# Performance work log

Measured on AMD Instinct MI355X. Metric: run time of the kernel, lower is better.

## Reference

```python
import jax, jax.numpy as jnp
from jax import lax
import numpy as np

B = 128      # graphs
L = 128      # nodes (tokens) per graph
N = B * L    # total nodes
E = 262144   # edges (avg degree 16)
VOCAB = 50000
EMB = 300
H = 256      # lstm hidden per direction
GCN = 512
NCLS = 2
EPS = 1e-12


def lstm_dir(x, wih, whh, b, reverse):
    # x: [B, L, EMB]; wih: [4H, EMB]; whh: [4H, H]; b: [4H]
    bsz, seq, _ = x.shape
    hdim = whh.shape[1]
    xs = jnp.einsum('ble,ge->blg', x, wih) + b  # [B, L, 4H]
    if reverse:
        xs = xs[:, ::-1]
    def step(carry, xt):
        h, c = carry
        gates = xt + h @ whh.T
        i, f, g, o = jnp.split(gates, 4, axis=-1)  # torch gate order i,f,g,o
        i = jax.nn.sigmoid(i); f = jax.nn.sigmoid(f)
        g = jnp.tanh(g); o = jax.nn.sigmoid(o)
        c = f * c + i * g
        h = o * jnp.tanh(c)
        return (h, c), h
    h0 = jnp.zeros((bsz, hdim), x.dtype)
    _, hs = lax.scan(step, (h0, h0), jnp.swapaxes(xs, 0, 1))
    hs = jnp.swapaxes(hs, 0, 1)  # [B, L, H]
    if reverse:
        hs = hs[:, ::-1]
    return hs


def sage_conv(x, src, dst, Wl, bl, Wr):
    # PyG SAGEConv(mean, normalize=True): lin_l(mean_j x_j) + lin_r(x_i), then L2-normalize
    msg = x[src]                                              # [E, d] gather
    agg = jax.ops.segment_sum(msg, dst, num_segments=x.shape[0])
    cnt = jax.ops.segment_sum(jnp.ones((src.shape[0], 1), x.dtype), dst,
                              num_segments=x.shape[0])
    agg = agg / jnp.maximum(cnt, 1.0)
    out = agg @ Wl + bl + x @ Wr
    nrm = jnp.linalg.norm(out, axis=-1, keepdims=True)
    return out / jnp.maximum(nrm, EPS)


def setup_inputs() -> dict:
    key = jax.random.key(0)
    ks = jax.random.split(key, 24)
    word_seq = jax.random.randint(ks[0], (B, L), 0, VOCAB)
    # intra-graph edges: local endpoints + graph offset
    el = jax.random.randint(ks[1], (2, E), 0, L)
    gid = jnp.repeat(jnp.arange(E // (E // B) * 0 + B), E // B)  # [E]
    edge_index = el + gid[None, :] * L
    batch = jnp.repeat(jnp.arange(B), L)
    s = 0.05
    inp = {
        'word_seq': word_seq, 'edge_index': edge_index, 'batch': batch,
        'embed_table': jax.random.normal(ks[2], (VOCAB, EMB), jnp.float32) * 0.1,
        'wih_f': jax.random.normal(ks[3], (4 * H, EMB), jnp.float32) * s,
        'whh_f': jax.random.normal(ks[4], (4 * H, H), jnp.float32) * s,
        'b_f': jax.random.normal(ks[5], (4 * H,), jnp.float32) * s,
        'wih_b': jax.random.normal(ks[6], (4 * H, EMB), jnp.float32) * s,
        'whh_b': jax.random.normal(ks[7], (4 * H, H), jnp.float32) * s,
        'b_b': jax.random.normal(ks[8], (4 * H,), jnp.float32) * s,
        'Wl1': jax.random.normal(ks[9], (2 * H, GCN), jnp.float32) * s,
        'Wr1': jax.random.normal(ks[10], (2 * H, GCN), jnp.float32) * s,
        'b1': jnp.zeros((GCN,), jnp.float32),
        'Wl2': jax.random.normal(ks[11], (GCN, 512), jnp.float32) * s,
        'Wr2': jax.random.normal(ks[12], (GCN, 512), jnp.float32) * s,
        'b2': jnp.zeros((512,), jnp.float32),
        'Wl3': jax.random.normal(ks[13], (512, 512), jnp.float32) * s,
        'Wr3': jax.random.normal(ks[14], (512, 512), jnp.float32) * s,
        'b3': jnp.zeros((512,), jnp.float32),
        'Wlin': jax.random.normal(ks[15], (512, NCLS), jnp.float32) * s,
        'blin': jnp.zeros((NCLS,), jnp.float32),
    }
    return inp


def reference(word_seq, edge_index, batch, embed_table,
              wih_f, whh_f, b_f, wih_b, whh_b, b_b,
              Wl1, Wr1, b1, Wl2, Wr2, b2, Wl3, Wr3, b3, Wlin, blin):
    # embedding (frozen) over padded per-graph sequences; uniform lengths -> plain reshape
    xe = embed_table[word_seq]                       # [B, L, EMB]
    hf = lstm_dir(xe, wih_f, whh_f, b_f, reverse=False)
    hb = lstm_dir(xe, wih_b, whh_b, b_b, reverse=True)
    x = jnp.concatenate([hf, hb], axis=-1).reshape(N, 2 * H)  # node features
    src, dst = edge_index[0], edge_index[1]
    x = jax.nn.relu(sage_conv(x, src, dst, Wl1, b1, Wr1))
    x = jax.nn.relu(sage_conv(x, src, dst, Wl2, b2, Wr2))
    x = jax.nn.relu(sage_conv(x, src, dst, Wl3, b3, Wr3))
    # global mean pool over graphs
    s = jax.ops.segment_sum(x, batch, num_segments=B)
    c = jax.ops.segment_sum(jnp.ones((N, 1), x.dtype), batch, num_segments=B)
    pooled = s / jnp.maximum(c, 1.0)
    return pooled @ Wlin + blin                      # [B, NCLS]
```

## Files before the change

### kernel.cpp

```cpp
#include <hip/hip_runtime.h>
#include <math.h>

#define NN   16384
#define EE   262144

typedef __attribute__((ext_vector_type(8))) short  short8v;
typedef __attribute__((ext_vector_type(4))) float  f32x4;

__device__ inline unsigned short f2bf(float f) {
    union { float f; unsigned u; } v; v.f = f;
    unsigned r = v.u + 0x7fff + ((v.u >> 16) & 1);
    return (unsigned short)(r >> 16);
}
__device__ inline float bf2f(unsigned short b) {
    unsigned u = ((unsigned)b) << 16;
    union { unsigned u; float f; } v; v.u = u; return v.f;
}
__device__ inline float sigm_f(float x) { return 1.f / (1.f + __expf(-x)); }
__device__ inline float tanh_f(float x) {
    x = fminf(15.f, fmaxf(-15.f, x));
    float e = __expf(2.f * x);
    return (e - 1.f) / (e + 1.f);
}
__device__ inline int gate_orig(int np) {
    int wp = np >> 6, g = (np >> 4) & 3, jj = np & 15;
    return g * 256 + wp * 16 + jj;
}

__global__ void k_init(unsigned long long* __restrict__ hx, int* __restrict__ deg,
                       int* __restrict__ fill) {
    int i = blockIdx.x * 256 + threadIdx.x;
    if (i < 65536) hx[i] = 0ull;
    if (i < NN) { deg[i] = 0; fill[i] = 0; }
}

__global__ void k_embed_bf(const int* __restrict__ wseq, const float* __restrict__ tab,
                           unsigned short* __restrict__ xeb) {
    int i = blockIdx.x * 256 + threadIdx.x;
    if (i >= NN * 320) return;
    int row = i / 320, k = i - row * 320;
    float f = (k < 300) ? tab[wseq[row] * 300 + k] : 0.f;
    xeb[i] = f2bf(f);
}

__global__ void k_cvt_wih(const float* __restrict__ wih, unsigned short* __restrict__ wt) {
    int i = blockIdx.x * 256 + threadIdx.x;
    if (i >= 1024 * 320) return;
    int np = i / 320, k = i - np * 320;
    wt[i] = f2bf(k < 300 ? wih[gate_orig(np) * 300 + k] : 0.f);
}
__global__ void k_cvt_whh(const float* __restrict__ whh, unsigned short* __restrict__ wp) {
    int i = blockIdx.x * 256 + threadIdx.x;
    if (i >= 1024 * 256) return;
    int np = i >> 8, k = i & 255;
    wp[i] = f2bf(whh[gate_orig(np) * 256 + k]);
}
__global__ void k_permb(const float* __restrict__ b, float* __restrict__ pb) {
    int i = blockIdx.x * 256 + threadIdx.x;
    if (i < 1024) pb[i] = b[gate_orig(i)];
}
__global__ void k_cvt_wcat(const float* __restrict__ Wl, const float* __restrict__ Wr,
                           unsigned short* __restrict__ wc) {
    int i = blockIdx.x * 256 + threadIdx.x;
    if (i >= 512 * 1024) return;
    int n = i >> 10, k = i & 1023;
    float f = (k < 512) ? Wl[k * 512 + n] : Wr[(k - 512) * 512 + n];
    wc[i] = f2bf(f);
}

__global__ __launch_bounds__(256)
void k_mgemm(const unsigned short* __restrict__ A, const unsigned short* __restrict__ Bt,
             const float* __restrict__ bias, float* __restrict__ C, int N, int Ka)
{
    __shared__ unsigned short As[128 * 32];
    __shared__ unsigned short Bs[128 * 32];
    const int tid = threadIdx.x;
    const int m0 = blockIdx.x << 7, n0 = blockIdx.y << 7;
    const int w = tid >> 6, lane = tid & 63;
    const int wr = w >> 1, wc = w & 1;
    const int lr = lane & 15, lhi = lane >> 4;
    const int r0 = tid >> 2, kc0 = (tid & 3) * 8;

    f32x4 acc[4][4] = {};

    for (int k0 = 0; k0 < Ka; k0 += 32) {
        short8v a0 = *(const short8v*)(A + (m0 + r0) * Ka + k0 + kc0);
        short8v a1 = *(const short8v*)(A + (m0 + 64 + r0) * Ka + k0 + kc0);
        short8v b0 = *(const short8v*)(Bt + (n0 + r0) * Ka + k0 + kc0);
        short8v b1 = *(const short8v*)(Bt + (n0 + 64 + r0) * Ka + k0 + kc0);
        __syncthreads();
        *(short8v*)&As[r0 * 32 + kc0]        = a0;
        *(short8v*)&As[(64 + r0) * 32 + kc0] = a1;
        *(short8v*)&Bs[r0 * 32 + kc0]        = b0;
        *(short8v*)&Bs[(64 + r0) * 32 + kc0] = b1;
        __syncthreads();
        short8v af[4], bf[4];
        #pragma unroll
        for (int i = 0; i < 4; ++i)
            af[i] = *(const short8v*)&As[(wr * 64 + i * 16 + lr) * 32 + lhi * 8];
        #pragma unroll
        for (int j = 0; j < 4; ++j)
            bf[j] = *(const short8v*)&Bs[(wc * 64 + j * 16 + lr) * 32 + lhi * 8];
        #pragma unroll
        for (int i = 0; i < 4; ++i)
            #pragma unroll
            for (int j = 0; j < 4; ++j)
                acc[i][j] = __builtin_amdgcn_mfma_f32_16x16x32_bf16(af[i], bf[j], acc[i][j], 0, 0, 0);
    }
    #pragma unroll
    for (int i = 0; i < 4; ++i) {
        int row = m0 + wr * 64 + i * 16 + lhi * 4;
        #pragma unroll
        for (int j = 0; j < 4; ++j) {
            int col = n0 + wc * 64 + j * 16 + lr;
            float bv = bias[col];
            #pragma unroll
            for (int r = 0; r < 4; ++r)
                C[(row + r) * N + col] = acc[i][j][r] + bv;
        }
    }
}

__global__ __launch_bounds__(512, 2)
void k_lstm(const float* __restrict__ xs_f, const float* __restrict__ xs_b,
            const unsigned short* __restrict__ whhp_f, const unsigned short* __restrict__ whhp_b,
            unsigned short* __restrict__ xout, unsigned long long* __restrict__ hx)
{
    const int tid  = threadIdx.x;
    const int wv   = tid >> 6, lane = tid & 63;
    const int lr   = lane & 15, lh = lane >> 4;
    const int wgid = blockIdx.x;
    const int dir  = wgid >> 4;
    const int bs   = (wgid >> 1) & 7;
    const int H    = wgid & 1;
    const int b0   = bs * 16;
    const float* xs = dir ? xs_b : xs_f;
    const unsigned short* whhp = dir ? whhp_b : whhp_f;

    short8v wf[4][8];
    #pragma unroll
    for (int g = 0; g < 4; ++g)
        #pragma unroll
        for (int ks = 0; ks < 8; ++ks)
            wf[g][ks] = *(const short8v*)(whhp
                + (size_t)(H * 512 + wv * 64 + g * 16 + lr) * 256 + ks * 32 + lh * 8);

    __shared__ unsigned short At[2][16 * 256];

    unsigned long long* hx_own =
        hx + (size_t)(((dir * 8 + bs) * 2 + H) * 2) * 1024;
    const unsigned long long* hx_peer =
        hx + (size_t)(((dir * 8 + bs) * 2 + (1 - H)) * 2) * 1024;

    const int jmine = H * 128 + wv * 16 + lr;
    const int rowb  = 4 * lh;
    const int up_j    = (1 - H) * 128 + (tid >> 2);
    const int up_rowb = 4 * (tid & 3);
    const int xcol    = H * 512 + wv * 64 + lr;

    float c[4] = {0.f, 0.f, 0.f, 0.f};
    float xv[4][4];
    {
        const int l0 = dir ? 127 : 0;
        #pragma unroll
        for (int r = 0; r < 4; ++r) {
            const float* xp = xs + ((size_t)(b0 + rowb + r) * 128 + l0) * 1024 + xcol;
            #pragma unroll
            for (int g = 0; g < 4; ++g) xv[g][r] = xp[g * 16];
        }
    }

    for (int t = 0; t < 128; ++t) {
        const int l = dir ? (127 - t) : t;
        f32x4 acc[4] = {};
        if (t > 0) {
            const char* Ab = (const char*)&At[(t - 1) & 1][0];
            #pragma unroll
            for (int ks = 0; ks < 8; ++ks) {
                int off = (lr * 512 + ks * 64 + lh * 16) ^ ((lr & 7) << 4);
                short8v a = *(const short8v*)(Ab + off);
                #pragma unroll
                for (int g = 0; g < 4; ++g)
                    acc[g] = __builtin_amdgcn_mfma_f32_16x16x32_bf16(a, wf[g][ks], acc[g], 0, 0, 0);
            }
        }
        unsigned short hb[4];
        #pragma unroll
        for (int r = 0; r < 4; ++r) {
            float gi = sigm_f(acc[0][r] + xv[0][r]);
            float gf = sigm_f(acc[1][r] + xv[1][r]);
            float gg = tanh_f(acc[2][r] + xv[2][r]);
            float go = sigm_f(acc[3][r] + xv[3][r]);
            c[r] = gf * c[r] + gi * gg;
            float h = go * tanh_f(c[r]);
            hb[r] = f2bf(h);
            xout[((size_t)(b0 + rowb + r) * 128 + l) * 512 + dir * 256 + jmine] = hb[r];
        }
        if (t < 127) {
            const int p = t & 1;
            char* Aw = (char*)&At[p][0];
            #pragma unroll
            for (int r = 0; r < 4; ++r) {
                int row = rowb + r;
                int off = (row * 512 + 2 * jmine) ^ ((row & 7) << 4);
                *(unsigned short*)(Aw + off) = hb[r];
            }
            const unsigned tg = (unsigned)(t + 1);
            unsigned long long w0 = ((unsigned long long)tg << 32)
                                  | ((unsigned)hb[0] | ((unsigned)hb[1] << 16));
            unsigned long long w1 = ((unsigned long long)tg << 32)
                                  | ((unsigned)hb[2] | ((unsigned)hb[3] << 16));
            const int Wb = (wv * 16 + lr) * 8 + 2 * lh;
            __hip_atomic_store(hx_own + (size_t)p * 1024 + Wb,     w0,
                               __ATOMIC_RELAXED, __HIP_MEMORY_SCOPE_AGENT);
            __hip_atomic_store(hx_own + (size_t)p * 1024 + Wb + 1, w1,
                               __ATOMIC_RELAXED, __HIP_MEMORY_SCOPE_AGENT);
            const int l2 = dir ? (126 - t) : (t + 1);
            #pragma unroll
            for (int r = 0; r < 4; ++r) {
                const float* xp = xs + ((size_t)(b0 + rowb + r) * 128 + l2) * 1024 + xcol;
                #pragma unroll
                for (int g = 0; g < 4; ++g) xv[g][r] = xp[g * 16];
            }
            const unsigned long long* pp = hx_peer + (size_t)p * 1024 + 2 * tid;
            unsigned long long u0 = __hip_atomic_load(pp,     __ATOMIC_RELAXED, __HIP_MEMORY_SCOPE_AGENT);
            unsigned long long u1 = __hip_atomic_load(pp + 1, __ATOMIC_RELAXED, __HIP_MEMORY_SCOPE_AGENT);
            while ((unsigned)(u0 >> 32) != tg)
                u0 = __hip_atomic_load(pp,     __ATOMIC_RELAXED, __HIP_MEMORY_SCOPE_AGENT);
            while ((unsigned)(u1 >> 32) != tg)
                u1 = __hip_atomic_load(pp + 1, __ATOMIC_RELAXED, __HIP_MEMORY_SCOPE_AGENT);
            {
                int r0_ = up_rowb, r1_ = up_rowb + 1, r2_ = up_rowb + 2, r3_ = up_rowb + 3;
                *(unsigned short*)(Aw + ((r0_ * 512 + 2 * up_j) ^ ((r0_ & 7) << 4))) =
                    (unsigned short)(u0 & 0xffff);
                *(unsigned short*)(Aw + ((r1_ * 512 + 2 * up_j) ^ ((r1_ & 7) << 4))) =
                    (unsigned short)((u0 >> 16) & 0xffff);
                *(unsigned short*)(Aw + ((r2_ * 512 + 2 * up_j) ^ ((r2_ & 7) << 4))) =
                    (unsigned short)(u1 & 0xffff);
                *(unsigned short*)(Aw + ((r3_ * 512 + 2 * up_j) ^ ((r3_ & 7) << 4))) =
                    (unsigned short)((u1 >> 16) & 0xffff);
            }
            __syncthreads();
        }
    }
}

__global__ void k_hist(const int* __restrict__ ei, int* __restrict__ deg) {
    int e = blockIdx.x * 256 + threadIdx.x;
    if (e >= EE) return;
    atomicAdd(&deg[ei[EE + e]], 1);
}

__global__ void k_scan(const int* __restrict__ deg, int* __restrict__ indptr) {
    __shared__ int sm[256];
    int tid = threadIdx.x;
    int b0 = tid * 64;
    int s = 0;
    for (int i = 0; i < 64; ++i) s += deg[b0 + i];
    sm[tid] = s;
    __syncthreads();
    for (int off = 1; off < 256; off <<= 1) {
        int v = (tid >= off) ? sm[tid - off] : 0;
        __syncthreads();
        sm[tid] += v;
        __syncthreads();
    }
    int run = sm[tid] - s;
    for (int i = 0; i < 64; ++i) { indptr[b0 + i] = run; run += deg[b0 + i]; }
    if (tid == 255) indptr[NN] = run;
}

__global__ void k_scatter(const int* __restrict__ ei, const int* __restrict__ indptr,
                          int* __restrict__ fill, int* __restrict__ cols) {
    int e = blockIdx.x * 256 + threadIdx.x;
    if (e >= EE) return;
    int d = ei[EE + e];
    int slot = atomicAdd(&fill[d], 1);
    cols[indptr[d] + slot] = ei[e];
}

__global__ __launch_bounds__(256)
void k_gather_bf(const unsigned short* __restrict__ x, const int* __restrict__ indptr,
                 const int* __restrict__ cols, unsigned short* __restrict__ catb)
{
    int gw = (blockIdx.x * 256 + threadIdx.x) >> 6;
    int lane = threadIdx.x & 63;
    if (gw >= NN) return;
    int s = indptr[gw], e = indptr[gw + 1];
    float a[8] = {};
    for (int p = s; p < e; ++p) {
        short8v v = *(const short8v*)(x + cols[p] * 512 + lane * 8);
        #pragma unroll
        for (int q = 0; q < 8; ++q) a[q] += bf2f((unsigned short)v[q]);
    }
    float sc = 1.f / (float)((e - s) > 1 ? (e - s) : 1);
    unsigned short* cp = catb + gw * 1024 + lane * 8;
    unsigned short o[8];
    #pragma unroll
    for (int q = 0; q < 8; ++q) o[q] = f2bf(a[q] * sc);
    *(short8v*)cp = *(short8v*)o;
    *(short8v*)(cp + 512) = *(const short8v*)(x + gw * 512 + lane * 8);
}

__global__ __launch_bounds__(256)
void k_norm_relu_bf(const float* __restrict__ y, unsigned short* __restrict__ o)
{
    int gw = (blockIdx.x * 256 + threadIdx.x) >> 6;
    int lane = threadIdx.x & 63;
    if (gw >= NN) return;
    const float* row = y + gw * 512 + lane * 8;
    float4 v0 = *(const float4*)row;
    float4 v1 = *(const float4*)(row + 4);
    float ss = v0.x*v0.x + v0.y*v0.y + v0.z*v0.z + v0.w*v0.w
             + v1.x*v1.x + v1.y*v1.y + v1.z*v1.z + v1.w*v1.w;
    #pragma unroll
    for (int off = 32; off >= 1; off >>= 1) ss += __shfl_xor(ss, off);
    float sc = 1.f / fmaxf(sqrtf(ss), 1e-12f);
    unsigned short ob[8];
    ob[0] = f2bf(fmaxf(v0.x*sc, 0.f)); ob[1] = f2bf(fmaxf(v0.y*sc, 0.f));
    ob[2] = f2bf(fmaxf(v0.z*sc, 0.f)); ob[3] = f2bf(fmaxf(v0.w*sc, 0.f));
    ob[4] = f2bf(fmaxf(v1.x*sc, 0.f)); ob[5] = f2bf(fmaxf(v1.y*sc, 0.f));
    ob[6] = f2bf(fmaxf(v1.z*sc, 0.f)); ob[7] = f2bf(fmaxf(v1.w*sc, 0.f));
    *(short8v*)(o + gw * 512 + lane * 8) = *(short8v*)ob;
}

__global__ __launch_bounds__(256)
void k_pool_bf(const unsigned short* __restrict__ x, const float* __restrict__ Wlin,
               const float* __restrict__ blin, float* __restrict__ out)
{
    int g = blockIdx.x;
    int tid = threadIdx.x;
    const unsigned short* base = x + (size_t)g * 128 * 512;
    float a0 = 0.f, a1 = 0.f;
    for (int r = 0; r < 128; ++r) {
        unsigned v = *(const unsigned*)(base + r * 512 + 2 * tid);
        a0 += bf2f((unsigned short)(v & 0xffff));
        a1 += bf2f((unsigned short)(v >> 16));
    }
    __shared__ float pooled[512];
    pooled[2*tid]     = a0 * (1.f / 128.f);
    pooled[2*tid + 1] = a1 * (1.f / 128.f);
    __syncthreads();
    if (tid < 64) {
        float p0 = 0.f, p1 = 0.f;
        for (int k = tid; k < 512; k += 64) {
            float pv = pooled[k];
            p0 += pv * Wlin[2*k];
            p1 += pv * Wlin[2*k + 1];
        }
        #pragma unroll
        for (int off = 32; off >= 1; off >>= 1) {
            p0 += __shfl_xor(p0, off);
            p1 += __shfl_xor(p1, off);
        }
        if (tid == 0) {
            out[2*g]     = p0 + blin[0];
            out[2*g + 1] = p1 + blin[1];
        }
    }
}

extern "C" void kernel_launch(void* const* d_in, const int* in_sizes, int n_in,
                              void* d_out, int out_size, void* d_ws, size_t ws_size,
                              hipStream_t stream)
{
    (void)in_sizes; (void)n_in; (void)out_size; (void)ws_size;
    const int*   word_seq = (const int*)  d_in[0];
    const int*   ei       = (const int*)  d_in[1];
    const float* tab      = (const float*)d_in[3];
    const float* wih_f    = (const float*)d_in[4];
    const float* whh_f    = (const float*)d_in[5];
    const float* b_f      = (const float*)d_in[6];
    const float* wih_b    = (const float*)d_in[7];
    const float* whh_b    = (const float*)d_in[8];
    const float* b_b      = (const float*)d_in[9];
    const float* Wl1      = (const float*)d_in[10];
    const float* Wr1      = (const float*)d_in[11];
    const float* b1       = (const float*)d_in[12];
    const float* Wl2      = (const float*)d_in[13];
    const float* Wr2      = (const float*)d_in[14];
    const float* b2       = (const float*)d_in[15];
    const float* Wl3      = (const float*)d_in[16];
    const float* Wr3      = (const float*)d_in[17];
    const float* b3       = (const float*)d_in[18];
    const float* Wlin     = (const float*)d_in[19];
    const float* blin     = (const float*)d_in[20];
    float* out = (float*)d_out;

    char* w = (char*)d_ws;
    int*   deg    = (int*)  (w);
    int*   indptr = (int*)  (w + 65536);
    int*   fill   = (int*)  (w + 131584);
    int*   cols   = (int*)  (w + 197120);
    unsigned long long* hx = (unsigned long long*)(w + 1245696);
    unsigned short* whhp_f = (unsigned short*)(w + 1769984);
    unsigned short* whhp_b = (unsigned short*)(w + 2294272);
    float* pb_f   = (float*)(w + 2818560);
    float* pb_b   = (float*)(w + 2822656);
    unsigned short* wt_f = (unsigned short*)(w + 2826752);
    unsigned short* wt_b = (unsigned short*)(w + 3482112);
    unsigned short* wc1  = (unsigned short*)(w + 4137472);
    unsigned short* wc2  = (unsigned short*)(w + 5186048);
    unsigned short* wc3  = (unsigned short*)(w + 6234624);
    unsigned short* xeb  = (unsigned short*)(w + 7283200);
    float* xs_f   = (float*)(w + 17768960);
    float* xs_b   = (float*)(w + 84877824);
    unsigned short* x0b = (unsigned short*)(w + 151986688);
    unsigned short* catb = (unsigned short*)(w + 17768960);
    float* x1     = (float*)(w + 51323392);
    unsigned short* xb_a = (unsigned short*)(w + 84877824);
    unsigned short* xb_b = (unsigned short*)(w + 101655040);

    k_embed_bf<<<20480, 256, 0, stream>>>(word_seq, tab, xeb);
    k_cvt_wih<<<1280, 256, 0, stream>>>(wih_f, wt_f);
    k_cvt_wih<<<1280, 256, 0, stream>>>(wih_b, wt_b);
    k_cvt_whh<<<1024, 256, 0, stream>>>(whh_f, whhp_f);
    k_cvt_whh<<<1024, 256, 0, stream>>>(whh_b, whhp_b);
    k_permb<<<4, 256, 0, stream>>>(b_f, pb_f);
    k_permb<<<4, 256, 0, stream>>>(b_b, pb_b);
    k_cvt_wcat<<<2048, 256, 0, stream>>>(Wl1, Wr1, wc1);
    k_cvt_wcat<<<2048, 256, 0, stream>>>(Wl2, Wr2, wc2);
    k_cvt_wcat<<<2048, 256, 0, stream>>>(Wl3, Wr3, wc3);

    k_init<<<256, 256, 0, stream>>>(hx, deg, fill);
    k_hist<<<1024, 256, 0, stream>>>(ei, deg);
    k_scan<<<1, 256, 0, stream>>>(deg, indptr);
    k_scatter<<<1024, 256, 0, stream>>>(ei, indptr, fill, cols);

    k_mgemm<<<dim3(128, 8), 256, 0, stream>>>(xeb, wt_f, pb_f, xs_f, 1024, 320);
    k_mgemm<<<dim3(128, 8), 256, 0, stream>>>(xeb, wt_b, pb_b, xs_b, 1024, 320);

    k_lstm<<<32, 512, 0, stream>>>(xs_f, xs_b, whhp_f, whhp_b, x0b, hx);

    k_gather_bf<<<4096, 256, 0, stream>>>(x0b, indptr, cols, catb);
    k_mgemm<<<dim3(128, 4), 256, 0, stream>>>(catb, wc1, b1, x1, 512, 1024);
    k_norm_relu_bf<<<4096, 256, 0, stream>>>(x1, xb_a);
    k_gather_bf<<<4096, 256, 0, stream>>>(xb_a, indptr, cols, catb);
    k_mgemm<<<dim3(128, 4), 256, 0, stream>>>(catb, wc2, b2, x1, 512, 1024);
    k_norm_relu_bf<<<4096, 256, 0, stream>>>(x1, xb_b);
    k_gather_bf<<<4096, 256, 0, stream>>>(xb_b, indptr, cols, catb);
    k_mgemm<<<dim3(128, 4), 256, 0, stream>>>(catb, wc3, b3, x1, 512, 1024);
    k_norm_relu_bf<<<4096, 256, 0, stream>>>(x1, xb_a);

    k_pool_bf<<<128, 256, 0, stream>>>(xb_a, Wlin, blin, out);
}
```

Measured before the change: 723.6 us.

## Interleave two batch slices per LSTM workgroup to hide peer-exchange latency

Each LSTM workgroup now handles two 16-row batch slices instead of one, halving the grid to 16 blocks. The two slices alternate within each timestep, so the cross-workgroup handshake of hidden-state halves for one slice overlaps with the MFMA and gate compute of the other. This targets the serial spin-wait latency in the recurrence. In exchange each block does twice the serial work per step and fewer CUs are used. The hx buffer layout is widened to four buffers per block, which depends on the init kernel clearing enough memory.

```diff
diff --git a/kernel.cpp b/kernel.cpp
--- a/kernel.cpp
+++ b/kernel.cpp
@@ -130,10 +130,9 @@
     const int wv   = tid >> 6, lane = tid & 63;
     const int lr   = lane & 15, lh = lane >> 4;
     const int wgid = blockIdx.x;
-    const int dir  = wgid >> 4;
-    const int bs   = (wgid >> 1) & 7;
+    const int dir  = wgid >> 3;
+    const int bs   = (wgid >> 1) & 3;
     const int H    = wgid & 1;
-    const int b0   = bs * 16;
     const float* xs = dir ? xs_b : xs_f;
     const unsigned short* whhp = dir ? whhp_b : whhp_f;
 
@@ -145,103 +144,172 @@
             wf[g][ks] = *(const short8v*)(whhp
                 + (size_t)(H * 512 + wv * 64 + g * 16 + lr) * 256 + ks * 32 + lh * 8);
 
-    __shared__ unsigned short At[2][16 * 256];
+    __shared__ unsigned short At[2][2][16 * 256];
 
     unsigned long long* hx_own =
-        hx + (size_t)(((dir * 8 + bs) * 2 + H) * 2) * 1024;
+        hx + (size_t)((dir * 4 + bs) * 2 + H) * 4096;
     const unsigned long long* hx_peer =
-        hx + (size_t)(((dir * 8 + bs) * 2 + (1 - H)) * 2) * 1024;
+        hx + (size_t)((dir * 4 + bs) * 2 + (1 - H)) * 4096;
 
     const int jmine = H * 128 + wv * 16 + lr;
     const int rowb  = 4 * lh;
     const int up_j    = (1 - H) * 128 + (tid >> 2);
     const int up_rowb = 4 * (tid & 3);
     const int xcol    = H * 512 + wv * 64 + lr;
-
-    float c[4] = {0.f, 0.f, 0.f, 0.f};
-    float xv[4][4];
+    const int Wb      = (wv * 16 + lr) * 8 + 2 * lh;
+    const int b0s0 = bs * 32, b0s1 = bs * 32 + 16;
+
+    float c0[4] = {0.f, 0.f, 0.f, 0.f};
+    float c1[4] = {0.f, 0.f, 0.f, 0.f};
+    float xv0[4][4], xv1[4][4];
     {
         const int l0 = dir ? 127 : 0;
         #pragma unroll
         for (int r = 0; r < 4; ++r) {
-            const float* xp = xs + ((size_t)(b0 + rowb + r) * 128 + l0) * 1024 + xcol;
+            const float* xp0 = xs + ((size_t)(b0s0 + rowb + r) * 128 + l0) * 1024 + xcol;
+            const float* xp1 = xs + ((size_t)(b0s1 + rowb + r) * 128 + l0) * 1024 + xcol;
             #pragma unroll
-            for (int g = 0; g < 4; ++g) xv[g][r] = xp[g * 16];
+            for (int g = 0; g < 4; ++g) { xv0[g][r] = xp0[g * 16]; xv1[g][r] = xp1[g * 16]; }
         }
     }
 
     for (int t = 0; t < 128; ++t) {
-        const int l = dir ? (127 - t) : t;
-        f32x4 acc[4] = {};
-        if (t > 0) {
-            const char* Ab = (const char*)&At[(t - 1) & 1][0];
-            #pragma unroll
-            for (int ks = 0; ks < 8; ++ks) {
-                int off = (lr * 512 + ks * 64 + lh * 16) ^ ((lr & 7) << 4);
-                short8v a = *(const short8v*)(Ab + off);
+        const int l  = dir ? (127 - t) : t;
+        const int l2 = dir ? (126 - t) : (t + 1);
+        const int p  = t & 1, q = p ^ 1;
+        const unsigned tg  = (unsigned)t;
+        const unsigned tg1 = (unsigned)(t + 1);
+
+        {
+            f32x4 acc[4] = {};
+            if (t > 0) {
+                const char* Ab = (const char*)&At[0][q][0];
                 #pragma unroll
-                for (int g = 0; g < 4; ++g)
-                    acc[g] = __builtin_amdgcn_mfma_f32_16x16x32_bf16(a, wf[g][ks], acc[g], 0, 0, 0);
+                for (int ks = 0; ks < 8; ++ks) {
+                    int off = (lr * 512 + ks * 64 + lh * 16) ^ ((lr & 7) << 4);
+                    short8v a = *(const short8v*)(Ab + off);
+                    #pragma unroll
+                    for (int g = 0; g < 4; ++g)
+                        acc[g] = __builtin_amdgcn_mfma_f32_16x16x32_bf16(a, wf[g][ks], acc[g], 0, 0, 0);
+                }
             }
-        }
-        unsigned short hb[4];
-        #pragma unroll
-        for (int r = 0; r < 4; ++r) {
-            float gi = sigm_f(acc[0][r] + xv[0][r]);
-            float gf = sigm_f(acc[1][r] + xv[1][r]);
-            float gg = tanh_f(acc[2][r] + xv[2][r]);
-            float go = sigm_f(acc[3][r] + xv[3][r]);
-            c[r] = gf * c[r] + gi * gg;
-            float h = go * tanh_f(c[r]);
-            hb[r] = f2bf(h);
-            xout[((size_t)(b0 + rowb + r) * 128 + l) * 512 + dir * 256 + jmine] = hb[r];
-        }
-        if (t < 127) {
-            const int p = t & 1;
-            char* Aw = (char*)&At[p][0];
+            unsigned short hb[4];
+            char* Aw = (char*)&At[0][p][0];
             #pragma unroll
             for (int r = 0; r < 4; ++r) {
+                float gi = sigm_f(acc[0][r] + xv0[0][r]);
+                float gf = sigm_f(acc[1][r] + xv0[1][r]);
+                float gg = tanh_f(acc[2][r] + xv0[2][r]);
+                float go = sigm_f(acc[3][r] + xv0[3][r]);
+                c0[r] = gf * c0[r] + gi * gg;
+                float h = go * tanh_f(c0[r]);
+                hb[r] = f2bf(h);
+                xout[((size_t)(b0s0 + rowb + r) * 128 + l) * 512 + dir * 256 + jmine] = hb[r];
                 int row = rowb + r;
-                int off = (row * 512 + 2 * jmine) ^ ((row & 7) << 4);
-                *(unsigned short*)(Aw + off) = hb[r];
+                *(unsigned short*)(Aw + ((row * 512 + 2 * jmine) ^ ((row & 7) << 4))) = hb[r];
             }
-            const unsigned tg = (unsigned)(t + 1);
-            unsigned long long w0 = ((unsigned long long)tg << 32)
-                                  | ((unsigned)hb[0] | ((unsigned)hb[1] << 16));
-            unsigned long long w1 = ((unsigned long long)tg << 32)
-                                  | ((unsigned)hb[2] | ((unsigned)hb[3] << 16));
-            const int Wb = (wv * 16 + lr) * 8 + 2 * lh;
-            __hip_atomic_store(hx_own + (size_t)p * 1024 + Wb,     w0,
-                               __ATOMIC_RELAXED, __HIP_MEMORY_SCOPE_AGENT);
-            __hip_atomic_store(hx_own + (size_t)p * 1024 + Wb + 1, w1,
-                               __ATOMIC_RELAXED, __HIP_MEMORY_SCOPE_AGENT);
-            const int l2 = dir ? (126 - t) : (t + 1);
-            #pragma unroll
-            for (int r = 0; r < 4; ++r) {
-                const float* xp = xs + ((size_t)(b0 + rowb + r) * 128 + l2) * 1024 + xcol;
+            if (t < 127) {
+                unsigned long long w0 = ((unsigned long long)tg1 << 32)
+                                      | ((unsigned)hb[0] | ((unsigned)hb[1] << 16));
+                unsigned long long w1 = ((unsigned long long)tg1 << 32)
+                                      | ((unsigned)hb[2] | ((unsigned)hb[3] << 16));
+                __hip_atomic_store(hx_own + (size_t)(0 * 2 + p) * 1024 + Wb,     w0,
+                                   __ATOMIC_RELAXED, __HIP_MEMORY_SCOPE_AGENT);
+                __hip_atomic_store(hx_own + (size_t)(0 * 2 + p) * 1024 + Wb + 1, w1,
+                                   __ATOMIC_RELAXED, __HIP_MEMORY_SCOPE_AGENT);
                 #pragma unroll
-                for (int g = 0; g < 4; ++g) xv[g][r] = xp[g * 16];
+                for (int r = 0; r < 4; ++r) {
+                    const float* xp = xs + ((size_t)(b0s0 + rowb + r) * 128 + l2) * 1024 + xcol;
+                    #pragma unroll
+                    for (int g = 0; g < 4; ++g) xv0[g][r] = xp[g * 16];
+                }
             }
-            const unsigned long long* pp = hx_peer + (size_t)p * 1024 + 2 * tid;
+        }
+        if (t > 0) {
+            const unsigned long long* pp = hx_peer + (size_t)(1 * 2 + q) * 1024 + 2 * tid;
             unsigned long long u0 = __hip_atomic_load(pp,     __ATOMIC_RELAXED, __HIP_MEMORY_SCOPE_AGENT);
             unsigned long long u1 = __hip_atomic_load(pp + 1, __ATOMIC_RELAXED, __HIP_MEMORY_SCOPE_AGENT);
             while ((unsigned)(u0 >> 32) != tg)
                 u0 = __hip_atomic_load(pp,     __ATOMIC_RELAXED, __HIP_MEMORY_SCOPE_AGENT);
             while ((unsigned)(u1 >> 32) != tg)
                 u1 = __hip_atomic_load(pp + 1, __ATOMIC_RELAXED, __HIP_MEMORY_SCOPE_AGENT);
-            {
-                int r0_ = up_rowb, r1_ = up_rowb + 1, r2_ = up_rowb + 2, r3_ = up_rowb + 3;
-                *(unsigned short*)(Aw + ((r0_ * 512 + 2 * up_j) ^ ((r0_ & 7) << 4))) =
-                    (unsigned short)(u0 & 0xffff);
-                *(unsigned short*)(Aw + ((r1_ * 512 + 2 * up_j) ^ ((r1_ & 7) << 4))) =
-                    (unsigned short)((u0 >> 16) & 0xffff);
-                *(unsigned short*)(Aw + ((r2_ * 512 + 2 * up_j) ^ ((r2_ & 7) << 4))) =
-                    (unsigned short)(u1 & 0xffff);
-                *(unsigned short*)(Aw + ((r3_ * 512 + 2 * up_j) ^ ((r3_ & 7) << 4))) =
-                    (unsigned short)((u1 >> 16) & 0xffff);
+            char* Aw = (char*)&At[1][q][0];
+            int r0_ = up_rowb, r1_ = up_rowb + 1, r2_ = up_rowb + 2, r3_ = up_rowb + 3;
+            *(unsigned short*)(Aw + ((r0_ * 512 + 2 * up_j) ^ ((r0_ & 7) << 4))) =
+                (unsigned short)(u0 & 0xffff);
+            *(unsigned short*)(Aw + ((r1_ * 512 + 2 * up_j) ^ ((r1_ & 7) << 4))) =
+                (unsigned short)((u0 >> 16) & 0xffff);
+            *(unsigned short*)(Aw + ((r2_ * 512 + 2 * up_j) ^ ((r2_ & 7) << 4))) =
+                (unsigned short)(u1 & 0xffff);
+            *(unsigned short*)(Aw + ((r3_ * 512 + 2 * up_j) ^ ((r3_ & 7) << 4))) =
+                (unsigned short)((u1 >> 16) & 0xffff);
+        }
+        __syncthreads();
+        {
+            f32x4 acc[4] = {};
+            if (t > 0) {
+                const char* Ab = (const char*)&At[1][q][0];
+                #pragma unroll
+                for (int ks = 0; ks < 8; ++ks) {
+                    int off = (lr * 512 + ks * 64 + lh * 16) ^ ((lr & 7) << 4);
+                    short8v a = *(const short8v*)(Ab + off);
+                    #pragma unroll
+                    for (int g = 0; g < 4; ++g)
+                        acc[g] = __builtin_amdgcn_mfma_f32_16x16x32_bf16(a, wf[g][ks], acc[g], 0, 0, 0);
+                }
             }
-            __syncthreads();
-        }
+            unsigned short hb[4];
+            char* Aw = (char*)&At[1][p][0];
+            #pragma unroll
+            for (int r = 0; r < 4; ++r) {
+                float gi = sigm_f(acc[0][r] + xv1[0][r]);
+                float gf = sigm_f(acc[1][r] + xv1[1][r]);
+                float gg = tanh_f(acc[2][r] + xv1[2][r]);
+                float go = sigm_f(acc[3][r] + xv1[3][r]);
+                c1[r] = gf * c1[r] + gi * gg;
+                float h = go * tanh_f(c1[r]);
+                hb[r] = f2bf(h);
+                xout[((size_t)(b0s1 + rowb + r) * 128 + l) * 512 + dir * 256 + jmine] = hb[r];
+                int row = rowb + r;
+                *(unsigned short*)(Aw + ((row * 512 + 2 * jmine) ^ ((row & 7) << 4))) = hb[r];
+            }
+            if (t < 127) {
+                unsigned long long w0 = ((unsigned long long)tg1 << 32)
+                                      | ((unsigned)hb[0] | ((unsigned)hb[1] << 16));
+                unsigned long long w1 = ((unsigned long long)tg1 << 32)
+                                      | ((unsigned)hb[2] | ((unsigned)hb[3] << 16));
+                __hip_atomic_store(hx_own + (size_t)(1 * 2 + p) * 1024 + Wb,     w0,
+                                   __ATOMIC_RELAXED, __HIP_MEMORY_SCOPE_AGENT);
+                __hip_atomic_store(hx_own + (size_t)(1 * 2 + p) * 1024 + Wb + 1, w1,
+                                   __ATOMIC_RELAXED, __HIP_MEMORY_SCOPE_AGENT);
+                #pragma unroll
+                for (int r = 0; r < 4; ++r) {
+                    const float* xp = xs + ((size_t)(b0s1 + rowb + r) * 128 + l2) * 1024 + xcol;
+                    #pragma unroll
+                    for (int g = 0; g < 4; ++g) xv1[g][r] = xp[g * 16];
+                }
+            }
+        }
+        if (t < 127) {
+            const unsigned long long* pp = hx_peer + (size_t)(0 * 2 + p) * 1024 + 2 * tid;
+            unsigned long long u0 = __hip_atomic_load(pp,     __ATOMIC_RELAXED, __HIP_MEMORY_SCOPE_AGENT);
+            unsigned long long u1 = __hip_atomic_load(pp + 1, __ATOMIC_RELAXED, __HIP_MEMORY_SCOPE_AGENT);
+            while ((unsigned)(u0 >> 32) != tg1)
+                u0 = __hip_atomic_load(pp,     __ATOMIC_RELAXED, __HIP_MEMORY_SCOPE_AGENT);
+            while ((unsigned)(u1 >> 32) != tg1)
+                u1 = __hip_atomic_load(pp + 1, __ATOMIC_RELAXED, __HIP_MEMORY_SCOPE_AGENT);
+            char* Aw = (char*)&At[0][p][0];
+            int r0_ = up_rowb, r1_ = up_rowb + 1, r2_ = up_rowb + 2, r3_ = up_rowb + 3;
+            *(unsigned short*)(Aw + ((r0_ * 512 + 2 * up_j) ^ ((r0_ & 7) << 4))) =
+                (unsigned short)(u0 & 0xffff);
+            *(unsigned short*)(Aw + ((r1_ * 512 + 2 * up_j) ^ ((r1_ & 7) << 4))) =
+                (unsigned short)((u0 >> 16) & 0xffff);
+            *(unsigned short*)(Aw + ((r2_ * 512 + 2 * up_j) ^ ((r2_ & 7) << 4))) =
+                (unsigned short)(u1 & 0xffff);
+            *(unsigned short*)(Aw + ((r3_ * 512 + 2 * up_j) ^ ((r3_ & 7) << 4))) =
+                (unsigned short)((u1 >> 16) & 0xffff);
+        }
+        __syncthreads();
     }
 }
 
@@ -430,7 +498,7 @@
     k_mgemm<<<dim3(128, 8), 256, 0, stream>>>(xeb, wt_f, pb_f, xs_f, 1024, 320);
     k_mgemm<<<dim3(128, 8), 256, 0, stream>>>(xeb, wt_b, pb_b, xs_b, 1024, 320);
 
-    k_lstm<<<32, 512, 0, stream>>>(xs_f, xs_b, whhp_f, whhp_b, x0b, hx);
+    k_lstm<<<16, 512, 0, stream>>>(xs_f, xs_b, whhp_f, whhp_b, x0b, hx);
 
     k_gather_bf<<<4096, 256, 0, stream>>>(x0b, indptr, cols, catb);
     k_mgemm<<<dim3(128, 4), 256, 0, stream>>>(catb, wc1, b1, x1, 512, 1024);
```

After: 1.039 ms. +43.5%, slower.

## Split LSTM recurrence across four workgroups per batch slice instead of two

Applied to the files above, without the earlier changes.

The recurrent LSTM kernel now splits each 16-row batch slice's hidden dimension across four cooperating workgroups (64 total) instead of two. Gate columns are re-permuted so each wave holds two MFMA tiles instead of four, and lanes swap gate values via shuffles to finish the elementwise update. This halves the per-step MFMA and register work per workgroup, at the cost of spinning on three peer workgroups' flag-tagged hidden-state exchanges per step instead of one. That adds cross-CU synchronization latency on the critical serial path.

```diff
diff --git a/kernel.cpp b/kernel.cpp
--- a/kernel.cpp
+++ b/kernel.cpp
@@ -22,9 +22,11 @@
     float e = __expf(2.f * x);
     return (e - 1.f) / (e + 1.f);
 }
-__device__ inline int gate_orig(int np) {
-    int wp = np >> 6, g = (np >> 4) & 3, jj = np & 15;
-    return g * 256 + wp * 16 + jj;
+__device__ inline int gate_orig2(int np) {
+    int Q = np >> 8, wv = (np >> 5) & 7, tile = (np >> 4) & 1, tc = np & 15;
+    int g = tile * 2 + (tc >> 3);
+    int j = Q * 64 + wv * 8 + (tc & 7);
+    return g * 256 + j;
 }
 
 __global__ void k_init(unsigned long long* __restrict__ hx, int* __restrict__ deg,
@@ -47,17 +49,17 @@
     int i = blockIdx.x * 256 + threadIdx.x;
     if (i >= 1024 * 320) return;
     int np = i / 320, k = i - np * 320;
-    wt[i] = f2bf(k < 300 ? wih[gate_orig(np) * 300 + k] : 0.f);
+    wt[i] = f2bf(k < 300 ? wih[gate_orig2(np) * 300 + k] : 0.f);
 }
 __global__ void k_cvt_whh(const float* __restrict__ whh, unsigned short* __restrict__ wp) {
     int i = blockIdx.x * 256 + threadIdx.x;
     if (i >= 1024 * 256) return;
     int np = i >> 8, k = i & 255;
-    wp[i] = f2bf(whh[gate_orig(np) * 256 + k]);
+    wp[i] = f2bf(whh[gate_orig2(np) * 256 + k]);
 }
 __global__ void k_permb(const float* __restrict__ b, float* __restrict__ pb) {
     int i = blockIdx.x * 256 + threadIdx.x;
-    if (i < 1024) pb[i] = b[gate_orig(i)];
+    if (i < 1024) pb[i] = b[gate_orig2(i)];
 }
 __global__ void k_cvt_wcat(const float* __restrict__ Wl, const float* __restrict__ Wr,
                            unsigned short* __restrict__ wc) {
@@ -128,117 +130,134 @@
 {
     const int tid  = threadIdx.x;
     const int wv   = tid >> 6, lane = tid & 63;
-    const int lr   = lane & 15, lh = lane >> 4;
+    const int lr16 = lane & 15, lh = lane >> 4;
+    const int b3   = (lane >> 3) & 1, lr3 = lane & 7;
     const int wgid = blockIdx.x;
-    const int dir  = wgid >> 4;
-    const int bs   = (wgid >> 1) & 7;
-    const int H    = wgid & 1;
+    const int dir  = wgid >> 5;
+    const int bs   = (wgid >> 2) & 7;
+    const int Q    = wgid & 3;
     const int b0   = bs * 16;
     const float* xs = dir ? xs_b : xs_f;
     const unsigned short* whhp = dir ? whhp_b : whhp_f;
 
-    short8v wf[4][8];
+    const int ncol0 = Q * 256 + wv * 32 + lr16;
+    short8v wf[2][8];
     #pragma unroll
-    for (int g = 0; g < 4; ++g)
+    for (int tt = 0; tt < 2; ++tt)
         #pragma unroll
         for (int ks = 0; ks < 8; ++ks)
-            wf[g][ks] = *(const short8v*)(whhp
-                + (size_t)(H * 512 + wv * 64 + g * 16 + lr) * 256 + ks * 32 + lh * 8);
+            wf[tt][ks] = *(const short8v*)(whhp
+                + (size_t)(ncol0 + tt * 16) * 256 + ks * 32 + lh * 8);
 
     __shared__ unsigned short At[2][16 * 256];
 
-    unsigned long long* hx_own =
-        hx + (size_t)(((dir * 8 + bs) * 2 + H) * 2) * 1024;
-    const unsigned long long* hx_peer =
-        hx + (size_t)(((dir * 8 + bs) * 2 + (1 - H)) * 2) * 1024;
-
-    const int jmine = H * 128 + wv * 16 + lr;
+    const int grpbase = (dir * 8 + bs) * 4 * 1024;
+    unsigned long long* hx_own = hx + grpbase + Q * 1024;
+
+    const int jmine = Q * 64 + wv * 8 + lr3;
     const int rowb  = 4 * lh;
-    const int up_j    = (1 - H) * 128 + (tid >> 2);
-    const int up_rowb = 4 * (tid & 3);
-    const int xcol    = H * 512 + wv * 64 + lr;
-
-    float c[4] = {0.f, 0.f, 0.f, 0.f};
-    float xv[4][4];
+    const int myr0  = rowb + 2 * b3;
+    const int up_jl = (tid >> 6) * 8 + (tid & 7);
+    const int up_r0 = 2 * ((tid >> 3) & 7);
+
+    float c0 = 0.f, c1 = 0.f;
+    float xv0[4], xv1[4];
     {
         const int l0 = dir ? 127 : 0;
         #pragma unroll
         for (int r = 0; r < 4; ++r) {
-            const float* xp = xs + ((size_t)(b0 + rowb + r) * 128 + l0) * 1024 + xcol;
-            #pragma unroll
-            for (int g = 0; g < 4; ++g) xv[g][r] = xp[g * 16];
+            const float* xp = xs + ((size_t)(b0 + rowb + r) * 128 + l0) * 1024;
+            xv0[r] = xp[ncol0];
+            xv1[r] = xp[ncol0 + 16];
         }
     }
 
     for (int t = 0; t < 128; ++t) {
         const int l = dir ? (127 - t) : t;
-        f32x4 acc[4] = {};
+        f32x4 acc0 = {}, acc1 = {};
         if (t > 0) {
             const char* Ab = (const char*)&At[(t - 1) & 1][0];
             #pragma unroll
             for (int ks = 0; ks < 8; ++ks) {
-                int off = (lr * 512 + ks * 64 + lh * 16) ^ ((lr & 7) << 4);
+                int off = (lr16 * 512 + ks * 64 + lh * 16) ^ ((lr16 & 7) << 4);
                 short8v a = *(const short8v*)(Ab + off);
-                #pragma unroll
-                for (int g = 0; g < 4; ++g)
-                    acc[g] = __builtin_amdgcn_mfma_f32_16x16x32_bf16(a, wf[g][ks], acc[g], 0, 0, 0);
+                acc0 = __builtin_amdgcn_mfma_f32_16x16x32_bf16(a, wf[0][ks], acc0, 0, 0, 0);
+                acc1 = __builtin_amdgcn_mfma_f32_16x16x32_bf16(a, wf[1][ks], acc1, 0, 0, 0);
             }
         }
-        unsigned short hb[4];
-        #pragma unroll
-        for (int r = 0; r < 4; ++r) {
-            float gi = sigm_f(acc[0][r] + xv[0][r]);
-            float gf = sigm_f(acc[1][r] + xv[1][r]);
-            float gg = tanh_f(acc[2][r] + xv[2][r]);
-            float go = sigm_f(acc[3][r] + xv[3][r]);
-            c[r] = gf * c[r] + gi * gg;
-            float h = go * tanh_f(c[r]);
-            hb[r] = f2bf(h);
-            xout[((size_t)(b0 + rowb + r) * 128 + l) * 512 + dir * 256 + jmine] = hb[r];
-        }
+        #pragma unroll
+        for (int r = 0; r < 4; ++r) { acc0[r] += xv0[r]; acc1[r] += xv1[r]; }
+        float z0 = b3 ? acc0[0] : acc0[2];
+        float z1 = b3 ? acc0[1] : acc0[3];
+        float z2 = b3 ? acc1[0] : acc1[2];
+        float z3 = b3 ? acc1[1] : acc1[3];
+        float y0 = __shfl_xor(z0, 8);
+        float y1 = __shfl_xor(z1, 8);
+        float y2 = __shfl_xor(z2, 8);
+        float y3 = __shfl_xor(z3, 8);
+        float iv0 = b3 ? y0 : acc0[0], iv1 = b3 ? y1 : acc0[1];
+        float fv0 = b3 ? acc0[2] : y0, fv1 = b3 ? acc0[3] : y1;
+        float gv0 = b3 ? y2 : acc1[0], gv1 = b3 ? y3 : acc1[1];
+        float ov0 = b3 ? acc1[2] : y2, ov1 = b3 ? acc1[3] : y3;
+        iv0 = sigm_f(iv0); fv0 = sigm_f(fv0); gv0 = tanh_f(gv0); ov0 = sigm_f(ov0);
+        c0 = fv0 * c0 + iv0 * gv0;
+        float h0 = ov0 * tanh_f(c0);
+        iv1 = sigm_f(iv1); fv1 = sigm_f(fv1); gv1 = tanh_f(gv1); ov1 = sigm_f(ov1);
+        c1 = fv1 * c1 + iv1 * gv1;
+        float h1 = ov1 * tanh_f(c1);
+        unsigned short hb0 = f2bf(h0), hb1 = f2bf(h1);
+        xout[((size_t)(b0 + myr0)     * 128 + l) * 512 + dir * 256 + jmine] = hb0;
+        xout[((size_t)(b0 + myr0 + 1) * 128 + l) * 512 + dir * 256 + jmine] = hb1;
+
         if (t < 127) {
             const int p = t & 1;
             char* Aw = (char*)&At[p][0];
-            #pragma unroll
-            for (int r = 0; r < 4; ++r) {
-                int row = rowb + r;
-                int off = (row * 512 + 2 * jmine) ^ ((row & 7) << 4);
-                *(unsigned short*)(Aw + off) = hb[r];
+            {
+                int r0_ = myr0, r1_ = myr0 + 1;
+                *(unsigned short*)(Aw + ((r0_ * 512 + 2 * jmine) ^ ((r0_ & 7) << 4))) = hb0;
+                *(unsigned short*)(Aw + ((r1_ * 512 + 2 * jmine) ^ ((r1_ & 7) << 4))) = hb1;
             }
             const unsigned tg = (unsigned)(t + 1);
-            unsigned long long w0 = ((unsigned long long)tg << 32)
-                                  | ((unsigned)hb[0] | ((unsigned)hb[1] << 16));
-            unsigned long long w1 = ((unsigned long long)tg << 32)
-                                  | ((unsigned)hb[2] | ((unsigned)hb[3] << 16));
-            const int Wb = (wv * 16 + lr) * 8 + 2 * lh;
-            __hip_atomic_store(hx_own + (size_t)p * 1024 + Wb,     w0,
-                               __ATOMIC_RELAXED, __HIP_MEMORY_SCOPE_AGENT);
-            __hip_atomic_store(hx_own + (size_t)p * 1024 + Wb + 1, w1,
+            unsigned long long w = ((unsigned long long)tg << 32)
+                                 | ((unsigned)hb0 | ((unsigned)hb1 << 16));
+            __hip_atomic_store(hx_own + p * 512 + tid, w,
                                __ATOMIC_RELAXED, __HIP_MEMORY_SCOPE_AGENT);
             const int l2 = dir ? (126 - t) : (t + 1);
             #pragma unroll
             for (int r = 0; r < 4; ++r) {
-                const float* xp = xs + ((size_t)(b0 + rowb + r) * 128 + l2) * 1024 + xcol;
-                #pragma unroll
-                for (int g = 0; g < 4; ++g) xv[g][r] = xp[g * 16];
+                const float* xp = xs + ((size_t)(b0 + rowb + r) * 128 + l2) * 1024;
+                xv0[r] = xp[ncol0];
+                xv1[r] = xp[ncol0 + 16];
             }
-            const unsigned long long* pp = hx_peer + (size_t)p * 1024 + 2 * tid;
-            unsigned long long u0 = __hip_atomic_load(pp,     __ATOMIC_RELAXED, __HIP_MEMORY_SCOPE_AGENT);
-            unsigned long long u1 = __hip_atomic_load(pp + 1, __ATOMIC_RELAXED, __HIP_MEMORY_SCOPE_AGENT);
-            while ((unsigned)(u0 >> 32) != tg)
-                u0 = __hip_atomic_load(pp,     __ATOMIC_RELAXED, __HIP_MEMORY_SCOPE_AGENT);
+            const unsigned long long* pp1 = hx + grpbase + (Q ^ 1) * 1024 + p * 512 + tid;
+            const unsigned long long* pp2 = hx + grpbase + (Q ^ 2) * 1024 + p * 512 + tid;
+            const unsigned long long* pp3 = hx + grpbase + (Q ^ 3) * 1024 + p * 512 + tid;
+            unsigned long long u1 = __hip_atomic_load(pp1, __ATOMIC_RELAXED, __HIP_MEMORY_SCOPE_AGENT);
+            unsigned long long u2 = __hip_atomic_load(pp2, __ATOMIC_RELAXED, __HIP_MEMORY_SCOPE_AGENT);
+            unsigned long long u3 = __hip_atomic_load(pp3, __ATOMIC_RELAXED, __HIP_MEMORY_SCOPE_AGENT);
             while ((unsigned)(u1 >> 32) != tg)
-                u1 = __hip_atomic_load(pp + 1, __ATOMIC_RELAXED, __HIP_MEMORY_SCOPE_AGENT);
+                u1 = __hip_atomic_load(pp1, __ATOMIC_RELAXED, __HIP_MEMORY_SCOPE_AGENT);
+            while ((unsigned)(u2 >> 32) != tg)
+                u2 = __hip_atomic_load(pp2, __ATOMIC_RELAXED, __HIP_MEMORY_SCOPE_AGENT);
+            while ((unsigned)(u3 >> 32) != tg)
+                u3 = __hip_atomic_load(pp3, __ATOMIC_RELAXED, __HIP_MEMORY_SCOPE_AGENT);
             {
-                int r0_ = up_rowb, r1_ = up_rowb + 1, r2_ = up_rowb + 2, r3_ = up_rowb + 3;
-                *(unsigned short*)(Aw + ((r0_ * 512 + 2 * up_j) ^ ((r0_ & 7) << 4))) =
-                    (unsigned short)(u0 & 0xffff);
-                *(unsigned short*)(Aw + ((r1_ * 512 + 2 * up_j) ^ ((r1_ & 7) << 4))) =
-                    (unsigned short)((u0 >> 16) & 0xffff);
-                *(unsigned short*)(Aw + ((r2_ * 512 + 2 * up_j) ^ ((r2_ & 7) << 4))) =
+                int ra = up_r0, rb = up_r0 + 1;
+                int j1 = (Q ^ 1) * 64 + up_jl;
+                int j2 = (Q ^ 2) * 64 + up_jl;
+                int j3 = (Q ^ 3) * 64 + up_jl;
+                *(unsigned short*)(Aw + ((ra * 512 + 2 * j1) ^ ((ra & 7) << 4))) =
                     (unsigned short)(u1 & 0xffff);
-                *(unsigned short*)(Aw + ((r3_ * 512 + 2 * up_j) ^ ((r3_ & 7) << 4))) =
+                *(unsigned short*)(Aw + ((rb * 512 + 2 * j1) ^ ((rb & 7) << 4))) =
                     (unsigned short)((u1 >> 16) & 0xffff);
+                *(unsigned short*)(Aw + ((ra * 512 + 2 * j2) ^ ((ra & 7) << 4))) =
+                    (unsigned short)(u2 & 0xffff);
+                *(unsigned short*)(Aw + ((rb * 512 + 2 * j2) ^ ((rb & 7) << 4))) =
+                    (unsigned short)((u2 >> 16) & 0xffff);
+                *(unsigned short*)(Aw + ((ra * 512 + 2 * j3) ^ ((ra & 7) << 4))) =
+                    (unsigned short)(u3 & 0xffff);
+                *(unsigned short*)(Aw + ((rb * 512 + 2 * j3) ^ ((rb & 7) << 4))) =
+                    (unsigned short)((u3 >> 16) & 0xffff);
             }
             __syncthreads();
         }
@@ -430,7 +449,7 @@
     k_mgemm<<<dim3(128, 8), 256, 0, stream>>>(xeb, wt_f, pb_f, xs_f, 1024, 320);
     k_mgemm<<<dim3(128, 8), 256, 0, stream>>>(xeb, wt_b, pb_b, xs_b, 1024, 320);
 
-    k_lstm<<<32, 512, 0, stream>>>(xs_f, xs_b, whhp_f, whhp_b, x0b, hx);
+    k_lstm<<<64, 512, 0, stream>>>(xs_f, xs_b, whhp_f, whhp_b, x0b, hx);
 
     k_gather_bf<<<4096, 256, 0, stream>>>(x0b, indptr, cols, catb);
     k_mgemm<<<dim3(128, 4), 256, 0, stream>>>(catb, wc1, b1, x1, 512, 1024);
```

New measurement: 653.3 us. -9.7%, faster.
